# Performance work log

Hardware: AMD Instinct MI355X
Metric: run time of the kernel (lower is better)

## Reference

```python
import jax, jax.numpy as jnp
import numpy as np

T, B, DIN, DH, NH = 256, 256, 1024, 1024, 16
HD = DH // NH


def setup_inputs() -> dict:
    key = jax.random.key(0)
    ks = jax.random.split(key, 11)
    w = lambda k, shape: jax.random.normal(k, shape, jnp.float32) * 0.02
    return {
        "inputs": jax.random.normal(ks[0], (T, B, DIN), jnp.float32),
        "Wg": w(ks[1], (4, DIN + DH, DH)),  # forget, input, update, output pre-gate linears
        "bg": w(ks[2], (4, DH)),
        "Wq": w(ks[3], (3, DH, DH)),  # forget, input, output attention gates
        "bq": w(ks[4], (3, DH)),
        "Wk": w(ks[5], (3, DH, DH)),
        "bk": w(ks[6], (3, DH)),
        "Wv": w(ks[7], (3, DH, DH)),
        "bv": w(ks[8], (3, DH)),
        "Wo": w(ks[9], (3, DH, DH)),
        "bo": w(ks[10], (3, DH)),
    }


def reference(inputs, Wg, bg, Wq, bq, Wk, bk, Wv, bv, Wo, bo):
    scale = 1.0 / np.sqrt(HD)
    sel = jnp.array([0, 1, 3])  # gates that use attention: forget, input, output

    def attn_gate(x):
        # x: [3, B, DH] -- three gate pre-activations processed in parallel
        q = (jnp.einsum('gbd,gde->gbe', x, Wq) + bq[:, None, :]).reshape(3, B, NH, HD)
        k = (jnp.einsum('gbd,gde->gbe', x, Wk) + bk[:, None, :]).reshape(3, B, NH, HD)
        v = (jnp.einsum('gbd,gde->gbe', x, Wv) + bv[:, None, :]).reshape(3, B, NH, HD)
        # attention ACROSS heads: [3, B, NH, NH]
        aw = jax.nn.softmax(jnp.einsum('gbhd,gbkd->gbhk', q, k) * scale, axis=-1)
        ao = jnp.einsum('gbhk,gbkd->gbhd', aw, v).reshape(3, B, DH)
        return jax.nn.sigmoid(jnp.einsum('gbd,gde->gbe', ao, Wo) + bo[:, None, :])

    def step(carry, x):
        hx, cx = carry
        comb = jnp.concatenate([x, hx], axis=1)          # [B, DIN+DH]
        pre = jnp.einsum('bi,gio->gbo', comb, Wg) + bg[:, None, :]  # [4, B, DH]
        f, i, o = attn_gate(pre[sel])                    # each [B, DH]
        g = jnp.tanh(pre[2])
        cx = f * cx + i * g
        hx = o * jnp.tanh(cx)
        return (hx, cx), hx

    init = (jnp.zeros((B, DH), inputs.dtype), jnp.zeros((B, DH), inputs.dtype))
    (hx, cx), outputs = jax.lax.scan(step, init, inputs)
    return outputs, hx, cx
```

## Files before the change

kernel.cpp:

```cpp
#include <hip/hip_runtime.h>

typedef __attribute__((ext_vector_type(8))) short bf8;
typedef __attribute__((ext_vector_type(8))) unsigned short us8;
typedef __attribute__((ext_vector_type(4))) unsigned short us4;
typedef __attribute__((ext_vector_type(4))) float f4;

#define NB 256
#define OUT_HX_OFF ((size_t)256 * 256 * 1024)
#define OUT_CX_OFF (OUT_HX_OFF + (size_t)256 * 1024)

static __device__ __forceinline__ unsigned short f2bf(float f) {
    unsigned u = __builtin_bit_cast(unsigned, f);
    return (unsigned short)((u + 0x7FFFu + ((u >> 16) & 1u)) >> 16);
}
static __device__ __forceinline__ float bf2f(unsigned short h) {
    return __builtin_bit_cast(float, (unsigned)h << 16);
}
static __device__ __forceinline__ float sigm(float x) {
    return 1.0f / (1.0f + __expf(-x));
}

#define MFMA16(a, b, c) __builtin_amdgcn_mfma_f32_16x16x32_bf16(a, b, c, 0, 0, 0)

#define GLDS16(g, l)                                                        \
    __builtin_amdgcn_global_load_lds(                                       \
        (const __attribute__((address_space(1))) void*)(g),                 \
        (__attribute__((address_space(3))) void*)(l), 16, 0, 0)

#define WAITV(n) asm volatile("s_waitcnt vmcnt(" #n ")" ::: "memory")
#define WAITL0 asm volatile("s_waitcnt lgkmcnt(0)" ::: "memory")
#define BARRIER                                                             \
    do {                                                                    \
        __builtin_amdgcn_s_barrier();                                       \
        __builtin_amdgcn_sched_barrier(0);                                  \
    } while (0)

template <int R>
static __device__ __forceinline__ void stage64(const unsigned short* g, int gstride,
                                               unsigned short* lds, int wave, int lane) {
#pragma unroll
    for (int j = 0; j < R / 32; ++j) {
        const int seg = wave * (R / 32) + j;
        const int row = seg * 8 + (lane >> 3);
        const int chunk = (lane & 7) ^ (row & 7);
        GLDS16(g + (size_t)row * gstride + chunk * 8, lds + seg * 512);
    }
}

static __device__ __forceinline__ bf8 fragld(const unsigned short* lds, int row, int ck) {
    return *(const bf8*)&lds[row * 64 + (((ck) ^ (row & 7)) << 3)];
}

__global__ __launch_bounds__(256) void k_x2bf(const float* __restrict__ src,
                                              unsigned short* __restrict__ dst, int n4) {
    const int stride = gridDim.x * 256;
    for (int i = blockIdx.x * 256 + threadIdx.x; i < n4; i += stride) {
        f4 v = ((const f4*)src)[i];
        us4 o;
        o[0] = f2bf(v[0]); o[1] = f2bf(v[1]); o[2] = f2bf(v[2]); o[3] = f2bf(v[3]);
        ((us4*)dst)[i] = o;
    }
}

__global__ __launch_bounds__(256) void k_transpose(const float* __restrict__ src,
                                                   unsigned short* __restrict__ dst,
                                                   int K, int N) {
    __shared__ float tile[32][33];
    const int tx = threadIdx.x & 31, ty = threadIdx.x >> 5;
    const int n0 = blockIdx.x * 32, k0 = blockIdx.y * 32;
#pragma unroll
    for (int i = 0; i < 4; ++i) tile[ty + i * 8][tx] = src[(size_t)(k0 + ty + i * 8) * N + n0 + tx];
    __syncthreads();
#pragma unroll
    for (int i = 0; i < 4; ++i)
        dst[(size_t)(n0 + ty + i * 8) * K + k0 + tx] = f2bf(tile[tx][ty + i * 8]);
}

__global__ __launch_bounds__(256) void k_xpre(const unsigned short* __restrict__ xbf,
                                              const unsigned short* __restrict__ wgT,
                                              const float* __restrict__ bg,
                                              unsigned short* __restrict__ xpre) {
    __shared__ unsigned short sA[2][128 * 64];
    __shared__ unsigned short sB[2][128 * 64];
    const int tid = threadIdx.x, lane = tid & 63, wave = tid >> 6;
    const int n0 = blockIdx.x * 128;
    const size_t m0 = (size_t)blockIdx.y * 128;
    const int wy = (wave >> 1) * 64, wx = (wave & 1) * 64;
    const int fr = lane & 15, fq = lane >> 4;
    f4 acc[4][4] = {};

    stage64<128>(xbf + m0 * 1024, 1024, sA[0], wave, lane);
    stage64<128>(wgT + (size_t)n0 * 2048, 2048, sB[0], wave, lane);
    WAITV(0); BARRIER;
#pragma unroll
    for (int i = 0; i < 16; ++i) {
        if (i + 1 < 16) {
            stage64<128>(xbf + m0 * 1024 + (i + 1) * 64, 1024, sA[(i + 1) & 1], wave, lane);
            stage64<128>(wgT + (size_t)n0 * 2048 + (i + 1) * 64, 2048, sB[(i + 1) & 1], wave, lane);
        }
        const unsigned short* A = sA[i & 1];
        const unsigned short* Bm = sB[i & 1];
#pragma unroll
        for (int ks = 0; ks < 2; ++ks) {
            bf8 af[4], bfv[4];
#pragma unroll
            for (int mi = 0; mi < 4; ++mi) af[mi] = fragld(A, wy + mi * 16 + fr, ks * 4 + fq);
#pragma unroll
            for (int ni = 0; ni < 4; ++ni) bfv[ni] = fragld(Bm, wx + ni * 16 + fr, ks * 4 + fq);
#pragma unroll
            for (int mi = 0; mi < 4; ++mi)
#pragma unroll
                for (int ni = 0; ni < 4; ++ni)
                    acc[mi][ni] = MFMA16(af[mi], bfv[ni], acc[mi][ni]);
        }
        if (i + 1 < 16) { WAITL0; WAITV(0); BARRIER; }
    }
#pragma unroll
    for (int mi = 0; mi < 4; ++mi)
#pragma unroll
        for (int ni = 0; ni < 4; ++ni) {
            const int col = n0 + wx + ni * 16 + fr;
            const float b = bg[col];
#pragma unroll
            for (int j = 0; j < 4; ++j) {
                const size_t row = m0 + wy + mi * 16 + fq * 4 + j;
                xpre[row * 4096 + col] = f2bf(acc[mi][ni][j] + b);
            }
        }
}

template <int XP>
__global__ __launch_bounds__(256, 2) void k_pre(
    const unsigned short* __restrict__ hxbf,
    const unsigned short* __restrict__ xt,
    const unsigned short* __restrict__ wgT,
    const float* __restrict__ bg,
    unsigned short* __restrict__ prebf,
    float* __restrict__ gupd) {
    __shared__ unsigned short sA[4][32 * 64];
    __shared__ unsigned short sB[4][64 * 64];
    const int tid = threadIdx.x, lane = tid & 63, wave = tid >> 6;
    const int n0 = blockIdx.x * 64, b0 = blockIdx.y * 32;
    const int wr = (wave & 1) * 16, wc = (wave >> 1) * 32;
    const int fr = lane & 15, fq = lane >> 4;
    constexpr int NT = XP ? 16 : 32;
    f4 acc[2] = {};

    const unsigned short* hb = hxbf + (size_t)b0 * 1024;
    const unsigned short* xb = xt + (XP ? 0 : (size_t)b0 * 1024);
    auto asrc = [&](int i) -> const unsigned short* {
        if (XP) return hb + i * 64;
        return i < 16 ? xb + i * 64 : hb + (i - 16) * 64;
    };
    auto bsrc = [&](int i) -> const unsigned short* {
        return wgT + (size_t)n0 * 2048 + (XP ? 1024 : 0) + i * 64;
    };

#pragma unroll
    for (int p = 0; p < 3; ++p) {
        stage64<32>(asrc(p), 1024, sA[p], wave, lane);
        stage64<64>(bsrc(p), 2048, sB[p], wave, lane);
    }
    WAITV(6); BARRIER;
#pragma unroll
    for (int i = 0; i < NT; ++i) {
        if (i + 3 < NT) {
            stage64<32>(asrc(i + 3), 1024, sA[(i + 3) & 3], wave, lane);
            stage64<64>(bsrc(i + 3), 2048, sB[(i + 3) & 3], wave, lane);
        }
        const unsigned short* A = sA[i & 3];
        const unsigned short* Bm = sB[i & 3];
#pragma unroll
        for (int ks = 0; ks < 2; ++ks) {
            bf8 a0 = fragld(A, wr + fr, ks * 4 + fq);
            bf8 b0v = fragld(Bm, wc + fr, ks * 4 + fq);
            bf8 b1v = fragld(Bm, wc + 16 + fr, ks * 4 + fq);
            acc[0] = MFMA16(a0, b0v, acc[0]);
            acc[1] = MFMA16(a0, b1v, acc[1]);
        }
        if (i < NT - 1) {
            WAITL0;
            if (i + 3 < NT) { WAITV(6); }
            else if (i + 2 < NT) { WAITV(3); }
            else { WAITV(0); }
            BARRIER;
        }
    }
#pragma unroll
    for (int ni = 0; ni < 2; ++ni) {
        const int col = n0 + wc + ni * 16 + fr;
        const int gg = col >> 10, d = col & 1023;
#pragma unroll
        for (int j = 0; j < 4; ++j) {
            const int row = b0 + wr + fq * 4 + j;
            float v = acc[ni][j];
            if (XP) v += bf2f(xt[(size_t)row * 4096 + col]);
            else v += bg[col];
            if (gg == 2) {
                gupd[(size_t)row * 1024 + d] = tanhf(v);
            } else {
                const int gm = (gg == 3) ? 2 : gg;
                prebf[((size_t)gm * NB + row) * 1024 + d] = f2bf(v);
            }
        }
    }
}

__global__ __launch_bounds__(256, 3) void k_qkv(
    const unsigned short* __restrict__ prebf,
    const unsigned short* __restrict__ wqkvT,
    const float* __restrict__ bq,
    const float* __restrict__ bk,
    const float* __restrict__ bv,
    unsigned short* __restrict__ qkvbf) {
    __shared__ unsigned short sA[4][32 * 64];
    __shared__ unsigned short sB[4][64 * 64];
    const int tid = threadIdx.x, lane = tid & 63, wave = tid >> 6;
    const int g = blockIdx.z;
    const int n0 = blockIdx.x * 64, b0 = blockIdx.y * 32;
    const unsigned short* Aab = prebf + ((size_t)g * NB + b0) * 1024;
    const unsigned short* Bb = wqkvT + ((size_t)g * 3072 + n0) * 1024;
    const int wr = (wave & 1) * 16, wc = (wave >> 1) * 32;
    const int fr = lane & 15, fq = lane >> 4;
    f4 acc[2] = {};

#pragma unroll
    for (int p = 0; p < 3; ++p) {
        stage64<32>(Aab + p * 64, 1024, sA[p], wave, lane);
        stage64<64>(Bb + p * 64, 1024, sB[p], wave, lane);
    }
    WAITV(6); BARRIER;
#pragma unroll
    for (int i = 0; i < 16; ++i) {
        if (i + 3 < 16) {
            stage64<32>(Aab + (i + 3) * 64, 1024, sA[(i + 3) & 3], wave, lane);
            stage64<64>(Bb + (i + 3) * 64, 1024, sB[(i + 3) & 3], wave, lane);
        }
        const unsigned short* A = sA[i & 3];
        const unsigned short* Bm = sB[i & 3];
#pragma unroll
        for (int ks = 0; ks < 2; ++ks) {
            bf8 a0 = fragld(A, wr + fr, ks * 4 + fq);
            bf8 b0v = fragld(Bm, wc + fr, ks * 4 + fq);
            bf8 b1v = fragld(Bm, wc + 16 + fr, ks * 4 + fq);
            acc[0] = MFMA16(a0, b0v, acc[0]);
            acc[1] = MFMA16(a0, b1v, acc[1]);
        }
        if (i < 15) {
            WAITL0;
            if (i + 3 < 16) { WAITV(6); }
            else if (i + 2 < 16) { WAITV(3); }
            else { WAITV(0); }
            BARRIER;
        }
    }
#pragma unroll
    for (int ni = 0; ni < 2; ++ni) {
        const int col = n0 + wc + ni * 16 + fr;
        const int which = col >> 10, d = col & 1023;
        const float* bp = which == 0 ? bq : (which == 1 ? bk : bv);
        const float bias = bp[g * 1024 + d];
#pragma unroll
        for (int j = 0; j < 4; ++j) {
            const int row = b0 + wr + fq * 4 + j;
            qkvbf[((size_t)g * NB + row) * 3072 + col] = f2bf(acc[ni][j] + bias);
        }
    }
}

__global__ __launch_bounds__(256) void k_attn(const unsigned short* __restrict__ qkvbf,
                                              unsigned short* __restrict__ aobf) {
    __shared__ unsigned short qs[16][72], ksm[16][72], vsm[16][72];
    __shared__ float aw[16][17];
    const int b = blockIdx.x, g = blockIdx.y, tid = threadIdx.x;
    const unsigned short* src = qkvbf + ((size_t)g * NB + b) * 3072;
#pragma unroll
    for (int j = 0; j < 3; ++j) {
        const int n = (j * 256 + tid) * 4;
        us4 dv = *(const us4*)(src + n);
        const int part = n >> 10, h = (n >> 6) & 15, c = n & 63;
        unsigned short* dst = part == 0 ? &qs[h][c] : (part == 1 ? &ksm[h][c] : &vsm[h][c]);
        *(us4*)dst = dv;
    }
    __syncthreads();
    const int h = tid >> 4, kp = tid & 15;
    float s = 0.f;
#pragma unroll
    for (int dblk = 0; dblk < 8; ++dblk) {
        us8 qv = *(const us8*)&qs[h][dblk * 8];
        us8 kv = *(const us8*)&ksm[kp][dblk * 8];
#pragma unroll
        for (int e = 0; e < 8; ++e) s += bf2f(qv[e]) * bf2f(kv[e]);
    }
    s *= 0.125f;
    float m = s;
#pragma unroll
    for (int off = 8; off; off >>= 1) m = fmaxf(m, __shfl_xor(m, off, 16));
    const float p = __expf(s - m);
    float sum = p;
#pragma unroll
    for (int off = 8; off; off >>= 1) sum += __shfl_xor(sum, off, 16);
    aw[h][kp] = p / sum;
    __syncthreads();
    float a0 = 0.f, a1 = 0.f, a2 = 0.f, a3 = 0.f;
#pragma unroll
    for (int kk = 0; kk < 16; ++kk) {
        const float w = aw[h][kk];
        us4 vv = *(const us4*)&vsm[kk][kp * 4];
        a0 += w * bf2f(vv[0]); a1 += w * bf2f(vv[1]);
        a2 += w * bf2f(vv[2]); a3 += w * bf2f(vv[3]);
    }
    us4 ov;
    ov[0] = f2bf(a0); ov[1] = f2bf(a1); ov[2] = f2bf(a2); ov[3] = f2bf(a3);
    *(us4*)(aobf + ((size_t)g * NB + b) * 1024 + h * 64 + kp * 4) = ov;
}

__global__ __launch_bounds__(256, 1) void k_gate(
    const unsigned short* __restrict__ aobf,
    const unsigned short* __restrict__ woT,
    const float* __restrict__ bo,
    const float* __restrict__ gupd,
    unsigned short* __restrict__ hxbf,
    float* __restrict__ out, int t) {
    __shared__ unsigned short sA[4][3][32 * 64];
    __shared__ unsigned short sB[4][3][32 * 64];
    const int tid = threadIdx.x, lane = tid & 63, wave = tid >> 6;
    const int d0 = blockIdx.x * 32, b0 = blockIdx.y * 32;
    const int wr = (wave & 1) * 16, wc = (wave >> 1) * 16;
    const int fr = lane & 15, fq = lane >> 4;
    f4 acc[3] = {};

    auto stage_all = [&](int i, int slot) {
#pragma unroll
        for (int g = 0; g < 3; ++g) {
            stage64<32>(aobf + ((size_t)g * NB + b0) * 1024 + i * 64, 1024,
                        sA[slot][g], wave, lane);
            stage64<32>(woT + ((size_t)g * 1024 + d0) * 1024 + i * 64, 1024,
                        sB[slot][g], wave, lane);
        }
    };

    stage_all(0, 0);
    stage_all(1, 1);
    stage_all(2, 2);
    WAITV(12); BARRIER;
#pragma unroll
    for (int i = 0; i < 16; ++i) {
        if (i + 3 < 16) stage_all(i + 3, (i + 3) & 3);
        const int sl = i & 3;
#pragma unroll
        for (int g = 0; g < 3; ++g) {
#pragma unroll
            for (int ks = 0; ks < 2; ++ks) {
                bf8 a0 = fragld(sA[sl][g], wr + fr, ks * 4 + fq);
                bf8 b0v = fragld(sB[sl][g], wc + fr, ks * 4 + fq);
                acc[g] = MFMA16(a0, b0v, acc[g]);
            }
        }
        if (i < 15) {
            WAITL0;
            if (i + 3 < 16) { WAITV(12); }
            else if (i + 2 < 16) { WAITV(6); }
            else { WAITV(0); }
            BARRIER;
        }
    }

    const int col = d0 + wc + fr;
    const float bof = bo[col], boi = bo[1024 + col], boo = bo[2048 + col];
    float* cxp = out + OUT_CX_OFF;
    float* hxp = out + OUT_HX_OFF;
    float* outs = out + (size_t)t * NB * 1024;
#pragma unroll
    for (int j = 0; j < 4; ++j) {
        const int row = b0 + wr + fq * 4 + j;
        const size_t idx = (size_t)row * 1024 + col;
        const float fg = sigm(acc[0][j] + bof);
        const float ig = sigm(acc[1][j] + boi);
        const float og = sigm(acc[2][j] + boo);
        const float c = fg * cxp[idx] + ig * gupd[idx];
        const float h = og * tanhf(c);
        cxp[idx] = c;
        hxp[idx] = h;
        outs[idx] = h;
        hxbf[idx] = f2bf(h);
    }
}

extern "C" void kernel_launch(void* const* d_in, const int* in_sizes, int n_in,
                              void* d_out, int out_size, void* d_ws, size_t ws_size,
                              hipStream_t stream) {
    const float* inputs = (const float*)d_in[0];
    const float* Wg = (const float*)d_in[1];
    const float* bg = (const float*)d_in[2];
    const float* Wq = (const float*)d_in[3];
    const float* bq = (const float*)d_in[4];
    const float* Wk = (const float*)d_in[5];
    const float* bk = (const float*)d_in[6];
    const float* Wv = (const float*)d_in[7];
    const float* bv = (const float*)d_in[8];
    const float* Wo = (const float*)d_in[9];
    const float* bo = (const float*)d_in[10];
    float* out = (float*)d_out;
    (void)in_sizes; (void)n_in; (void)out_size;

    char* ws = (char*)d_ws;
    size_t off = 0;
    auto alloc = [&](size_t bytes) -> void* {
        void* p = ws + off;
        off += (bytes + 255) & ~(size_t)255;
        return p;
    };
    unsigned short* wgT   = (unsigned short*)alloc((size_t)4096 * 2048 * 2);
    unsigned short* wqkvT = (unsigned short*)alloc((size_t)3 * 3072 * 1024 * 2);
    unsigned short* woT   = (unsigned short*)alloc((size_t)3 * 1024 * 1024 * 2);
    unsigned short* hxbf  = (unsigned short*)alloc((size_t)256 * 1024 * 2);
    unsigned short* prebf = (unsigned short*)alloc((size_t)3 * 256 * 1024 * 2);
    float*          gupd  = (float*)alloc((size_t)256 * 1024 * 4);
    unsigned short* qkvbf = (unsigned short*)alloc((size_t)3 * 256 * 3072 * 2);
    unsigned short* aobf  = (unsigned short*)alloc((size_t)3 * 256 * 1024 * 2);
    unsigned short* xbfs  = (unsigned short*)alloc((size_t)2 * 256 * 1024 * 2);
    const size_t off_base = off;
    unsigned short* xbf   = (unsigned short*)alloc((size_t)65536 * 1024 * 2);
    const size_t off_t2 = off;
    unsigned short* xpre  = (unsigned short*)alloc((size_t)65536 * 4096 * 2);
    const size_t off_t1 = off;

    const int tier = (ws_size >= off_t1) ? 1 : (ws_size >= off_t2 ? 2 : 3);
    if (ws_size < off_base) return;

    hipMemsetAsync(hxbf, 0, (size_t)256 * 1024 * 2, stream);
    hipMemsetAsync(out + OUT_CX_OFF, 0, (size_t)256 * 1024 * 4, stream);

    for (int g = 0; g < 4; ++g)
        k_transpose<<<dim3(32, 64), 256, 0, stream>>>(
            Wg + (size_t)g * 2048 * 1024, wgT + (size_t)g * 1024 * 2048, 2048, 1024);
    const float* wsrc[3] = {Wq, Wk, Wv};
    for (int g = 0; g < 3; ++g)
        for (int wi = 0; wi < 3; ++wi)
            k_transpose<<<dim3(32, 32), 256, 0, stream>>>(
                wsrc[wi] + (size_t)g * 1024 * 1024,
                wqkvT + (size_t)g * 3072 * 1024 + (size_t)wi * 1024 * 1024, 1024, 1024);
    for (int g = 0; g < 3; ++g)
        k_transpose<<<dim3(32, 32), 256, 0, stream>>>(
            Wo + (size_t)g * 1024 * 1024, woT + (size_t)g * 1024 * 1024, 1024, 1024);

    if (tier <= 2) k_x2bf<<<2048, 256, 0, stream>>>(inputs, xbf, 16777216);
    if (tier == 1) k_xpre<<<dim3(32, 512), 256, 0, stream>>>(xbf, wgT, bg, xpre);

    for (int t = 0; t < 256; ++t) {
        if (tier == 3)
            k_x2bf<<<64, 256, 0, stream>>>(inputs + (size_t)t * 262144,
                                           xbfs + (size_t)(t & 1) * 262144, 65536);
        if (tier == 1)
            k_pre<1><<<dim3(64, 8), 256, 0, stream>>>(
                hxbf, xpre + (size_t)t * 256 * 4096, wgT, bg, prebf, gupd);
        else
            k_pre<0><<<dim3(64, 8), 256, 0, stream>>>(
                hxbf,
                tier == 2 ? xbf + (size_t)t * 262144 : xbfs + (size_t)(t & 1) * 262144,
                wgT, bg, prebf, gupd);
        k_qkv<<<dim3(48, 8, 3), 256, 0, stream>>>(prebf, wqkvT, bq, bk, bv, qkvbf);
        k_attn<<<dim3(256, 3), 256, 0, stream>>>(qkvbf, aobf);
        k_gate<<<dim3(32, 8), 256, 0, stream>>>(aobf, woT, bo, gupd, hxbf, out, t);
    }
}
```

Baseline: 13.33 ms.

## Fold gate pre-linear into QKV weights to remove per-step pre-GEMM

```diff
diff --git a/kernel.cpp b/kernel.cpp
--- a/kernel.cpp
+++ b/kernel.cpp
@@ -74,6 +74,146 @@
 #pragma unroll
     for (int i = 0; i < 4; ++i)
         dst[(size_t)(n0 + ty + i * 8) * K + k0 + tx] = f2bf(tile[tx][ty + i * 8]);
+}
+
+__global__ __launch_bounds__(256) void k_wf(const unsigned short* __restrict__ Aab,
+                                            const unsigned short* __restrict__ Bb,
+                                            unsigned short* __restrict__ outp,
+                                            int outstride) {
+    __shared__ unsigned short sA[2][128 * 64];
+    __shared__ unsigned short sB[2][128 * 64];
+    const int tid = threadIdx.x, lane = tid & 63, wave = tid >> 6;
+    const int n0 = blockIdx.x * 128, m0 = blockIdx.y * 128;
+    const int wy = (wave >> 1) * 64, wx = (wave & 1) * 64;
+    const int fr = lane & 15, fq = lane >> 4;
+    f4 acc[4][4] = {};
+
+    stage64<128>(Aab + (size_t)m0 * 1024, 1024, sA[0], wave, lane);
+    stage64<128>(Bb + (size_t)n0 * 1024, 1024, sB[0], wave, lane);
+    WAITV(0); BARRIER;
+#pragma unroll
+    for (int i = 0; i < 16; ++i) {
+        if (i + 1 < 16) {
+            stage64<128>(Aab + (size_t)m0 * 1024 + (i + 1) * 64, 1024, sA[(i + 1) & 1], wave, lane);
+            stage64<128>(Bb + (size_t)n0 * 1024 + (i + 1) * 64, 1024, sB[(i + 1) & 1], wave, lane);
+        }
+        const unsigned short* A = sA[i & 1];
+        const unsigned short* Bm = sB[i & 1];
+#pragma unroll
+        for (int ks = 0; ks < 2; ++ks) {
+            bf8 af[4], bfv[4];
+#pragma unroll
+            for (int mi = 0; mi < 4; ++mi) af[mi] = fragld(A, wy + mi * 16 + fr, ks * 4 + fq);
+#pragma unroll
+            for (int ni = 0; ni < 4; ++ni) bfv[ni] = fragld(Bm, wx + ni * 16 + fr, ks * 4 + fq);
+#pragma unroll
+            for (int mi = 0; mi < 4; ++mi)
+#pragma unroll
+                for (int ni = 0; ni < 4; ++ni)
+                    acc[mi][ni] = MFMA16(af[mi], bfv[ni], acc[mi][ni]);
+        }
+        if (i + 1 < 16) { WAITL0; WAITV(0); BARRIER; }
+    }
+#pragma unroll
+    for (int mi = 0; mi < 4; ++mi)
+#pragma unroll
+        for (int ni = 0; ni < 4; ++ni) {
+            const int col = n0 + wx + ni * 16 + fr;
+#pragma unroll
+            for (int j = 0; j < 4; ++j) {
+                const int row = m0 + wy + mi * 16 + fq * 4 + j;
+                outp[(size_t)row * outstride + col] = f2bf(acc[mi][ni][j]);
+            }
+        }
+}
+
+__global__ __launch_bounds__(256) void k_seg9(const unsigned short* __restrict__ wgT,
+                                              unsigned short* __restrict__ wbigX,
+                                              unsigned short* __restrict__ wbigH) {
+    const int d = blockIdx.x, k4 = threadIdx.x * 4;
+    us4 vx = *(const us4*)(wgT + (size_t)(2048 + d) * 2048 + k4);
+    us4 vh = *(const us4*)(wgT + (size_t)(2048 + d) * 2048 + 1024 + k4);
+    *(us4*)(wbigX + (size_t)(9216 + d) * 1024 + k4) = vx;
+    *(us4*)(wbigH + (size_t)(9216 + d) * 1024 + k4) = vh;
+}
+
+__global__ __launch_bounds__(256) void k_cbig(const float* __restrict__ bg,
+                                              const float* __restrict__ Wq,
+                                              const float* __restrict__ Wk,
+                                              const float* __restrict__ Wv,
+                                              const float* __restrict__ bq,
+                                              const float* __restrict__ bk,
+                                              const float* __restrict__ bv,
+                                              float* __restrict__ cbig) {
+    const int n = blockIdx.x * 256 + threadIdx.x;
+    const int j = n >> 10, d = n & 1023;
+    float s;
+    if (j < 9) {
+        const int gp = j / 3, which = j % 3;
+        const int selg = (gp == 2) ? 3 : gp;
+        const float* W = which == 0 ? Wq : (which == 1 ? Wk : Wv);
+        const float* bqkv = which == 0 ? bq : (which == 1 ? bk : bv);
+        s = bqkv[gp * 1024 + d];
+        const float* wb = W + (size_t)gp * 1024 * 1024;
+        const float* bgb = bg + selg * 1024;
+        for (int k = 0; k < 1024; ++k) s += bgb[k] * wb[(size_t)k * 1024 + d];
+    } else {
+        s = bg[2048 + d];
+    }
+    cbig[n] = s;
+}
+
+__global__ __launch_bounds__(256) void k_xbig(const unsigned short* __restrict__ xbf,
+                                              const unsigned short* __restrict__ wbigX,
+                                              const float* __restrict__ cbig,
+                                              unsigned short* __restrict__ XBIG) {
+    __shared__ unsigned short sA[2][128 * 64];
+    __shared__ unsigned short sB[2][128 * 64];
+    const int tid = threadIdx.x, lane = tid & 63, wave = tid >> 6;
+    const int n0 = blockIdx.x * 128;
+    const size_t m0 = (size_t)blockIdx.y * 128;
+    const int wy = (wave >> 1) * 64, wx = (wave & 1) * 64;
+    const int fr = lane & 15, fq = lane >> 4;
+    f4 acc[4][4] = {};
+
+    stage64<128>(xbf + m0 * 1024, 1024, sA[0], wave, lane);
+    stage64<128>(wbigX + (size_t)n0 * 1024, 1024, sB[0], wave, lane);
+    WAITV(0); BARRIER;
+#pragma unroll
+    for (int i = 0; i < 16; ++i) {
+        if (i + 1 < 16) {
+            stage64<128>(xbf + m0 * 1024 + (i + 1) * 64, 1024, sA[(i + 1) & 1], wave, lane);
+            stage64<128>(wbigX + (size_t)n0 * 1024 + (i + 1) * 64, 1024, sB[(i + 1) & 1], wave, lane);
+        }
+        const unsigned short* A = sA[i & 1];
+        const unsigned short* Bm = sB[i & 1];
+#pragma unroll
+        for (int ks = 0; ks < 2; ++ks) {
+            bf8 af[4], bfv[4];
+#pragma unroll
+            for (int mi = 0; mi < 4; ++mi) af[mi] = fragld(A, wy + mi * 16 + fr, ks * 4 + fq);
+#pragma unroll
+            for (int ni = 0; ni < 4; ++ni) bfv[ni] = fragld(Bm, wx + ni * 16 + fr, ks * 4 + fq);
+#pragma unroll
+            for (int mi = 0; mi < 4; ++mi)
+#pragma unroll
+                for (int ni = 0; ni < 4; ++ni)
+                    acc[mi][ni] = MFMA16(af[mi], bfv[ni], acc[mi][ni]);
+        }
+        if (i + 1 < 16) { WAITL0; WAITV(0); BARRIER; }
+    }
+#pragma unroll
+    for (int mi = 0; mi < 4; ++mi)
+#pragma unroll
+        for (int ni = 0; ni < 4; ++ni) {
+            const int col = n0 + wx + ni * 16 + fr;
+            const float b = cbig[col];
+#pragma unroll
+            for (int j = 0; j < 4; ++j) {
+                const size_t row = m0 + wy + mi * 16 + fq * 4 + j;
+                XBIG[row * 10240 + col] = f2bf(acc[mi][ni][j] + b);
+            }
+        }
 }
 
 __global__ __launch_bounds__(256) void k_xpre(const unsigned short* __restrict__ xbf,
@@ -127,6 +267,70 @@
                 xpre[row * 4096 + col] = f2bf(acc[mi][ni][j] + b);
             }
         }
+}
+
+__global__ __launch_bounds__(256, 3) void k_qg(
+    const unsigned short* __restrict__ hxbf,
+    const unsigned short* __restrict__ wbigH,
+    const unsigned short* __restrict__ XBIGt,
+    unsigned short* __restrict__ qkvbf,
+    float* __restrict__ gupd) {
+    __shared__ unsigned short sA[4][32 * 64];
+    __shared__ unsigned short sB[4][64 * 64];
+    const int tid = threadIdx.x, lane = tid & 63, wave = tid >> 6;
+    const int n0 = blockIdx.x * 64, b0 = blockIdx.y * 32;
+    const unsigned short* Aab = hxbf + (size_t)b0 * 1024;
+    const unsigned short* Bb = wbigH + (size_t)n0 * 1024;
+    const int wr = (wave & 1) * 16, wc = (wave >> 1) * 32;
+    const int fr = lane & 15, fq = lane >> 4;
+    f4 acc[2] = {};
+
+#pragma unroll
+    for (int p = 0; p < 3; ++p) {
+        stage64<32>(Aab + p * 64, 1024, sA[p], wave, lane);
+        stage64<64>(Bb + p * 64, 1024, sB[p], wave, lane);
+    }
+    WAITV(6); BARRIER;
+#pragma unroll
+    for (int i = 0; i < 16; ++i) {
+        if (i + 3 < 16) {
+            stage64<32>(Aab + (i + 3) * 64, 1024, sA[(i + 3) & 3], wave, lane);
+            stage64<64>(Bb + (i + 3) * 64, 1024, sB[(i + 3) & 3], wave, lane);
+        }
+        const unsigned short* A = sA[i & 3];
+        const unsigned short* Bm = sB[i & 3];
+#pragma unroll
+        for (int ks = 0; ks < 2; ++ks) {
+            bf8 a0 = fragld(A, wr + fr, ks * 4 + fq);
+            bf8 b0v = fragld(Bm, wc + fr, ks * 4 + fq);
+            bf8 b1v = fragld(Bm, wc + 16 + fr, ks * 4 + fq);
+            acc[0] = MFMA16(a0, b0v, acc[0]);
+            acc[1] = MFMA16(a0, b1v, acc[1]);
+        }
+        if (i < 15) {
+            WAITL0;
+            if (i + 3 < 16) { WAITV(6); }
+            else if (i + 2 < 16) { WAITV(3); }
+            else { WAITV(0); }
+            BARRIER;
+        }
+    }
+#pragma unroll
+    for (int ni = 0; ni < 2; ++ni) {
+        const int col = n0 + wc + ni * 16 + fr;
+        const int seg = col >> 10, d = col & 1023;
+#pragma unroll
+        for (int j = 0; j < 4; ++j) {
+            const int row = b0 + wr + fq * 4 + j;
+            const float v = acc[ni][j] + bf2f(XBIGt[(size_t)row * 10240 + col]);
+            if (seg == 9) {
+                gupd[(size_t)row * 1024 + d] = tanhf(v);
+            } else {
+                const int gp = seg / 3, which = seg % 3;
+                qkvbf[((size_t)gp * NB + row) * 3072 + which * 1024 + d] = f2bf(v);
+            }
+        }
+    }
 }
 
 template <int XP>
@@ -414,6 +618,7 @@
     unsigned short* wgT   = (unsigned short*)alloc((size_t)4096 * 2048 * 2);
     unsigned short* wqkvT = (unsigned short*)alloc((size_t)3 * 3072 * 1024 * 2);
     unsigned short* woT   = (unsigned short*)alloc((size_t)3 * 1024 * 1024 * 2);
+    unsigned short* wgnt  = (unsigned short*)alloc((size_t)4 * 2048 * 1024 * 2);
     unsigned short* hxbf  = (unsigned short*)alloc((size_t)256 * 1024 * 2);
     unsigned short* prebf = (unsigned short*)alloc((size_t)3 * 256 * 1024 * 2);
     float*          gupd  = (float*)alloc((size_t)256 * 1024 * 4);
@@ -422,12 +627,21 @@
     unsigned short* xbfs  = (unsigned short*)alloc((size_t)2 * 256 * 1024 * 2);
     const size_t off_base = off;
     unsigned short* xbf   = (unsigned short*)alloc((size_t)65536 * 1024 * 2);
-    const size_t off_t2 = off;
-    unsigned short* xpre  = (unsigned short*)alloc((size_t)65536 * 4096 * 2);
-    const size_t off_t1 = off;
-
-    const int tier = (ws_size >= off_t1) ? 1 : (ws_size >= off_t2 ? 2 : 3);
-    if (ws_size < off_base) return;
+    const size_t off_xbf = off;
+    unsigned short* wbigX = (unsigned short*)alloc((size_t)10240 * 1024 * 2);
+    unsigned short* wbigH = (unsigned short*)alloc((size_t)10240 * 1024 * 2);
+    float*          cbig  = (float*)alloc((size_t)10240 * 4);
+    unsigned short* XBIG  = (unsigned short*)alloc((size_t)65536 * 10240 * 2);
+    const size_t off_tF = off;
+    unsigned short* xpre  = wbigX;
+    const size_t off_t1 = off_xbf + (((size_t)65536 * 4096 * 2 + 255) & ~(size_t)255);
+
+    int tier;
+    if (ws_size >= off_tF) tier = 0;
+    else if (ws_size >= off_t1) tier = 1;
+    else if (ws_size >= off_xbf) tier = 2;
+    else if (ws_size >= off_base) tier = 3;
+    else return;
 
     hipMemsetAsync(hxbf, 0, (size_t)256 * 1024 * 2, stream);
     hipMemsetAsync(out + OUT_CX_OFF, 0, (size_t)256 * 1024 * 4, stream);
@@ -446,22 +660,48 @@
             Wo + (size_t)g * 1024 * 1024, woT + (size_t)g * 1024 * 1024, 1024, 1024);
 
     if (tier <= 2) k_x2bf<<<2048, 256, 0, stream>>>(inputs, xbf, 16777216);
-    if (tier == 1) k_xpre<<<dim3(32, 512), 256, 0, stream>>>(xbf, wgT, bg, xpre);
-
-    for (int t = 0; t < 256; ++t) {
-        if (tier == 3)
-            k_x2bf<<<64, 256, 0, stream>>>(inputs + (size_t)t * 262144,
-                                           xbfs + (size_t)(t & 1) * 262144, 65536);
-        if (tier == 1)
-            k_pre<1><<<dim3(64, 8), 256, 0, stream>>>(
-                hxbf, xpre + (size_t)t * 256 * 4096, wgT, bg, prebf, gupd);
-        else
-            k_pre<0><<<dim3(64, 8), 256, 0, stream>>>(
-                hxbf,
-                tier == 2 ? xbf + (size_t)t * 262144 : xbfs + (size_t)(t & 1) * 262144,
-                wgT, bg, prebf, gupd);
-        k_qkv<<<dim3(48, 8, 3), 256, 0, stream>>>(prebf, wqkvT, bq, bk, bv, qkvbf);
-        k_attn<<<dim3(256, 3), 256, 0, stream>>>(qkvbf, aobf);
-        k_gate<<<dim3(32, 8), 256, 0, stream>>>(aobf, woT, bo, gupd, hxbf, out, t);
-    }
-}
+
+    if (tier == 0) {
+        k_x2bf<<<2048, 256, 0, stream>>>(Wg, wgnt, 2097152);
+        for (int gp = 0; gp < 3; ++gp) {
+            const int selg = (gp == 2) ? 3 : gp;
+            for (int which = 0; which < 3; ++which) {
+                const int j = gp * 3 + which;
+                const unsigned short* A =
+                    wqkvT + ((size_t)gp * 3072 + which * 1024) * 1024;
+                const unsigned short* Bx = wgnt + (size_t)selg * 2048 * 1024;
+                const unsigned short* Bh = Bx + (size_t)1024 * 1024;
+                k_wf<<<dim3(8, 8), 256, 0, stream>>>(A, Bx, wbigX + (size_t)j * 1024 * 1024, 1024);
+                k_wf<<<dim3(8, 8), 256, 0, stream>>>(A, Bh, wbigH + (size_t)j * 1024 * 1024, 1024);
+            }
+        }
+        k_seg9<<<1024, 256, 0, stream>>>(wgT, wbigX, wbigH);
+        k_cbig<<<40, 256, 0, stream>>>(bg, Wq, Wk, Wv, bq, bk, bv, cbig);
+        k_xbig<<<dim3(80, 512), 256, 0, stream>>>(xbf, wbigX, cbig, XBIG);
+
+        for (int t = 0; t < 256; ++t) {
+            k_qg<<<dim3(160, 8), 256, 0, stream>>>(
+                hxbf, wbigH, XBIG + (size_t)t * 256 * 10240, qkvbf, gupd);
+            k_attn<<<dim3(256, 3), 256, 0, stream>>>(qkvbf, aobf);
+            k_gate<<<dim3(32, 8), 256, 0, stream>>>(aobf, woT, bo, gupd, hxbf, out, t);
+        }
+    } else {
+        if (tier == 1) k_xpre<<<dim3(32, 512), 256, 0, stream>>>(xbf, wgT, bg, xpre);
+        for (int t = 0; t < 256; ++t) {
+            if (tier == 3)
+                k_x2bf<<<64, 256, 0, stream>>>(inputs + (size_t)t * 262144,
+                                               xbfs + (size_t)(t & 1) * 262144, 65536);
+            if (tier == 1)
+                k_pre<1><<<dim3(64, 8), 256, 0, stream>>>(
+                    hxbf, xpre + (size_t)t * 256 * 4096, wgT, bg, prebf, gupd);
+            else
+                k_pre<0><<<dim3(64, 8), 256, 0, stream>>>(
+                    hxbf,
+                    tier == 2 ? xbf + (size_t)t * 262144 : xbfs + (size_t)(t & 1) * 262144,
+                    wgT, bg, prebf, gupd);
+            k_qkv<<<dim3(48, 8, 3), 256, 0, stream>>>(prebf, wqkvT, bq, bk, bv, qkvbf);
+            k_attn<<<dim3(256, 3), 256, 0, stream>>>(qkvbf, aobf);
+            k_gate<<<dim3(32, 8), 256, 0, stream>>>(aobf, woT, bo, gupd, hxbf, out, t);
+        }
+    }
+}
```

Measured after the change: 13.32 ms. No clear change (-0.0%).
